# Kernel tuning notes

Hardware: AMD Instinct MI355X
Metric: run time of the kernel (lower is better)

Reference implementation:

```python
import jax, jax.numpy as jnp
import numpy as np

N, T, D, H = 4, 2048, 512, 8
HD = D // H  # head dim = split size


def setup_inputs() -> dict:
    key = jax.random.key(0)
    k1, k2, k3, k4 = jax.random.split(key, 4)
    scale = 1.0 / np.sqrt(D)
    return {
        "query": jax.random.normal(k1, (N, T, D), dtype=jnp.float32),
        "Wk": jax.random.normal(k2, (D, D), dtype=jnp.float32) * scale,
        "Wv": jax.random.normal(k3, (D, D), dtype=jnp.float32) * scale,
        "Wo": jax.random.normal(k4, (D, D), dtype=jnp.float32) * scale,
    }


def reference(query, Wk, Wv, Wo):
    # torch.nn.Linear(x) == x @ W.T (no bias)
    querys = query                              # [N, T, D]
    keys = query @ Wk.T + query                 # residual-added keys [N, T, D]
    values = query @ Wv.T                       # [N, T, D]

    # split along feature dim into H heads, stacked on a leading head axis
    def split_heads(x):
        # [N, T, D] -> [H, N, T, HD]
        return jnp.transpose(x.reshape(N, T, H, HD), (2, 0, 1, 3))

    q = split_heads(querys)
    k = split_heads(keys)
    v = split_heads(values)

    scores = jnp.einsum("hnqd,hnkd->hnqk", q, k) / np.sqrt(HD).astype(np.float32)
    scores = jax.nn.softmax(scores, axis=3)      # [H, N, Tq, Tk]
    out = jnp.einsum("hnqk,hnkd->hnqd", scores, v)

    # concat heads back along feature dim: [H, N, T, HD] -> [N, T, D]
    out = jnp.transpose(out, (1, 2, 0, 3)).reshape(N, T, D)
    out = out @ Wo.T
    return out
```

## Files before the change

kernel.cpp:

```cpp
#include <hip/hip_runtime.h>
#include <cstdint>
#include <cstddef>

#define NB 4
#define TS 2048
#define DM 512
#define HN 8
#define HD 64

typedef __attribute__((ext_vector_type(8))) short bf16x8;
typedef __attribute__((ext_vector_type(16))) float f32x16;
typedef __attribute__((ext_vector_type(4))) float f32x4;
typedef __attribute__((ext_vector_type(4))) short short4v;
typedef __attribute__((ext_vector_type(4))) unsigned u32x4;

static __device__ __forceinline__ short f2bf(float f) {
  unsigned u = __float_as_uint(f);
  unsigned r = (u + 0x7fffu + ((u >> 16) & 1u)) >> 16;
  return (short)r;
}

static __device__ __forceinline__ float bf2f(short s) {
  return __uint_as_float(((unsigned)(unsigned short)s) << 16);
}

static __device__ __forceinline__ unsigned cvtpk(float lo, float hi) {
  unsigned r;
  asm("v_cvt_pk_bf16_f32 %0, %1, %2" : "=v"(r) : "v"(lo), "v"(hi));
  return r;
}

static __device__ __forceinline__ void plane32swap(unsigned& x, unsigned& y) {
  asm volatile("v_permlane32_swap_b32 %0, %1" : "+v"(x), "+v"(y));
}

static __device__ __forceinline__ void gload16(const void* g, void* l) {
  __builtin_amdgcn_global_load_lds(
      (const __attribute__((address_space(1))) void*)g,
      (__attribute__((address_space(3))) void*)l, 16, 0, 0);
}

#define WAIT_VM(N) asm volatile("s_waitcnt vmcnt(" #N ")" ::: "memory")
#define BAR() __builtin_amdgcn_s_barrier()

#define MFMA16(a, b, c) __builtin_amdgcn_mfma_f32_16x16x32_bf16((a), (b), (c), 0, 0, 0)
#define MFMA32(a, b, c) __builtin_amdgcn_mfma_f32_32x32x16_bf16((a), (b), (c), 0, 0, 0)

__global__ __launch_bounds__(256) void cast_all(const float* __restrict__ Q,
                                                const float* __restrict__ Wk,
                                                const float* __restrict__ Wv,
                                                const float* __restrict__ Wo,
                                                short* __restrict__ Qb,
                                                short* __restrict__ Wb) {
  int i = blockIdx.x * 256 + threadIdx.x;
  const int Q4 = (NB * TS * DM) / 4;
  const float* src;
  short* dst;
  int off;
  if (i < Q4) {
    src = Q; dst = Qb; off = i;
  } else {
    int j = i - Q4;
    int which = j >> 16;
    off = j & 65535;
    src = which == 0 ? Wk : (which == 1 ? Wv : Wo);
    dst = Wb + ((size_t)which << 18);
  }
  float4 v = reinterpret_cast<const float4*>(src)[off];
  short4v o;
  o.x = f2bf(v.x);
  o.y = f2bf(v.y);
  o.z = f2bf(v.z);
  o.w = f2bf(v.w);
  reinterpret_cast<short4v*>(dst)[off] = o;
}

template <int MODE>
__global__ __launch_bounds__(256) void gemm512(const short* __restrict__ A,
                                               const short* __restrict__ W,
                                               const float* __restrict__ resid,
                                               void* __restrict__ out0) {
  __shared__ alignas(16) short lA[2][128 * 32];
  __shared__ alignas(16) short lB[2][64 * 32];
  const int row0 = blockIdx.x * 128;
  const int col0 = blockIdx.y * 64;
  const int tid = threadIdx.x;
  const int lane = tid & 63;
  const int wave = tid >> 6;
  const int wr = wave >> 1, wc = wave & 1;
  const int fr = lane & 15, fk = (lane >> 4) * 8;

  f32x4 acc[4][2];
  const f32x4 z4 = {0.f, 0.f, 0.f, 0.f};
#pragma unroll
  for (int m = 0; m < 4; ++m)
#pragma unroll
    for (int nn = 0; nn < 2; ++nn) acc[m][nn] = z4;

  const int sr = tid >> 2;
  const int sc8 = (tid & 3) * 8;

#define GSTAGE(buf, kt)                                                \
  do {                                                                 \
    gload16(&A[(size_t)(row0 + sr) * DM + (kt) + sc8],                 \
            (char*)&lA[(buf)][0] + (size_t)tid * 16);                  \
    gload16(&A[(size_t)(row0 + 64 + sr) * DM + (kt) + sc8],            \
            (char*)&lA[(buf)][0] + 4096 + (size_t)tid * 16);           \
    gload16(&W[(size_t)(col0 + sr) * DM + (kt) + sc8],                 \
            (char*)&lB[(buf)][0] + (size_t)tid * 16);                  \
  } while (0)

  GSTAGE(0, 0);
  __syncthreads();
  int cur = 0;
  for (int kt = 0; kt < 16; ++kt) {
    if (kt < 15) GSTAGE(cur ^ 1, (kt + 1) * 32);
    bf16x8 af[4], bfr[2];
#pragma unroll
    for (int m = 0; m < 4; ++m)
      af[m] = *reinterpret_cast<const bf16x8*>(&lA[cur][(wr * 64 + m * 16 + fr) * 32 + fk]);
#pragma unroll
    for (int nn = 0; nn < 2; ++nn)
      bfr[nn] = *reinterpret_cast<const bf16x8*>(&lB[cur][(wc * 32 + nn * 16 + fr) * 32 + fk]);
    __builtin_amdgcn_s_setprio(1);
#pragma unroll
    for (int m = 0; m < 4; ++m)
#pragma unroll
      for (int nn = 0; nn < 2; ++nn) acc[m][nn] = MFMA16(af[m], bfr[nn], acc[m][nn]);
    __builtin_amdgcn_s_setprio(0);
    __syncthreads();
    cur ^= 1;
  }
#undef GSTAGE

#pragma unroll
  for (int m = 0; m < 4; ++m) {
#pragma unroll
    for (int nn = 0; nn < 2; ++nn) {
#pragma unroll
      for (int i = 0; i < 4; ++i) {
        int gr = row0 + wr * 64 + m * 16 + (lane >> 4) * 4 + i;
        int gc = col0 + wc * 32 + nn * 16 + fr;
        float v = acc[m][nn][i];
        if (MODE == 0) {
          v += resid[(size_t)gr * DM + gc];
          reinterpret_cast<short*>(out0)[(size_t)gr * DM + gc] = f2bf(v);
        } else if (MODE == 1) {
          int nb = gc >> 11, t = gc & (TS - 1);
          reinterpret_cast<short*>(out0)[((size_t)nb * DM + gr) * TS + t] = f2bf(v);
        } else {
          reinterpret_cast<float*>(out0)[(size_t)gr * DM + gc] = v;
        }
      }
    }
  }
}

__global__ __launch_bounds__(512, 4) void attn(const short* __restrict__ Qb,
                                               const short* __restrict__ Kb,
                                               const short* __restrict__ Vt,
                                               short* __restrict__ Ob) {
  __shared__ alignas(16) short kv[2][2][64 * 64];
  const int bid = blockIdx.x;
  const int blk = (bid & 7) * 64 + (bid >> 3);
  const int qt = blk & 15;
  const int nh = blk >> 4;
  const int h = nh & (HN - 1);
  const int n = nh >> 3;
  const int wv = threadIdx.x >> 6, lane = threadIdx.x & 63;
  const int grp = wv >> 2, qs = wv & 3;
  const int l31 = lane & 31, hf = lane >> 5;
  const int q0 = qt * 128 + qs * 32;
  const float SC2 = 0.18033688011f;

  bf16x8 qf[4];
  const short* qrow = Qb + (size_t)(n * TS + q0 + l31) * DM + h * HD;
#pragma unroll
  for (int ks = 0; ks < 4; ++ks) {
    bf16x8 t = *reinterpret_cast<const bf16x8*>(qrow + ks * 16 + hf * 8);
#pragma unroll
    for (int j = 0; j < 8; ++j) t[j] = f2bf(bf2f(t[j]) * SC2);
    qf[ks] = t;
  }

  bf16x8 ones;
#pragma unroll
  for (int i = 0; i < 8; ++i) ones[i] = (short)0x3F80;

  f32x16 o0, o1, osum;
#pragma unroll
  for (int r = 0; r < 16; ++r) {
    o0[r] = 0.f;
    o1[r] = 0.f;
    osum[r] = 0.f;
  }

  const int srow8 = lane >> 3;
  const int scol = ((lane & 7) ^ srow8) * 8;
  const int swz = (l31 & 7) << 4;
  const int tbase = grp * 16;

#define STAGE(t)                                                                      \
  do {                                                                                \
    int r0_ = qs * 16 + srow8;                                                        \
    int r1_ = r0_ + 8;                                                                \
    char* kb_ = (char*)&kv[grp][0][0] + qs * 2048;                                    \
    char* vb_ = (char*)&kv[grp][1][0] + qs * 2048;                                    \
    gload16(Kb + (size_t)(n * TS + (t) * 64 + r0_) * DM + h * HD + scol, kb_);        \
    gload16(Kb + (size_t)(n * TS + (t) * 64 + r1_) * DM + h * HD + scol, kb_ + 1024); \
    gload16(Vt + ((size_t)(nh * HD + r0_) * TS + (t) * 64 + scol), vb_);              \
    gload16(Vt + ((size_t)(nh * HD + r1_) * TS + (t) * 64 + scol), vb_ + 1024);       \
  } while (0)

  STAGE(tbase);

  for (int j = 0; j < 16; ++j) {
    WAIT_VM(0);
    BAR();

    const char* Kl = (const char*)&kv[grp][0][0];
    const char* Vl = (const char*)&kv[grp][1][0];

    f32x16 s0, s1;
#pragma unroll
    for (int r = 0; r < 16; ++r) {
      s0[r] = 0.f;
      s1[r] = 0.f;
    }
    __builtin_amdgcn_s_setprio(1);
#pragma unroll
    for (int ks = 0; ks < 4; ++ks) {
      int colb = ks * 32 + hf * 16;
      bf16x8 ka0 = *reinterpret_cast<const bf16x8*>(Kl + l31 * 128 + (colb ^ swz));
      bf16x8 ka1 = *reinterpret_cast<const bf16x8*>(Kl + (l31 + 32) * 128 + (colb ^ swz));
      s0 = MFMA32(ka0, qf[ks], s0);
      s1 = MFMA32(ka1, qf[ks], s1);
    }
    __builtin_amdgcn_s_setprio(0);

#pragma unroll
    for (int r = 0; r < 16; ++r) {
      s0[r] = __builtin_amdgcn_exp2f(s0[r]);
      s1[r] = __builtin_amdgcn_exp2f(s1[r]);
    }

    unsigned w0[4][2], w1[4][2];
#pragma unroll
    for (int c = 0; c < 4; ++c) {
      w0[c][0] = cvtpk(s0[4 * c], s0[4 * c + 1]);
      w0[c][1] = cvtpk(s0[4 * c + 2], s0[4 * c + 3]);
      w1[c][0] = cvtpk(s1[4 * c], s1[4 * c + 1]);
      w1[c][1] = cvtpk(s1[4 * c + 2], s1[4 * c + 3]);
    }

    __builtin_amdgcn_s_setprio(1);
#pragma unroll
    for (int ks = 0; ks < 4; ++ks) {
      const int ce = (ks & 1) * 2, co = ce + 1;
      unsigned xa = (ks < 2) ? w0[ce][0] : w1[ce][0];
      unsigned xb = (ks < 2) ? w0[ce][1] : w1[ce][1];
      unsigned ya = (ks < 2) ? w0[co][0] : w1[co][0];
      unsigned yb = (ks < 2) ? w0[co][1] : w1[co][1];
      plane32swap(xa, ya);
      plane32swap(xb, yb);
      u32x4 pw;
      pw.x = xa;
      pw.y = xb;
      pw.z = ya;
      pw.w = yb;
      bf16x8 pa = *reinterpret_cast<bf16x8*>(&pw);

      int colb = ks * 32 + hf * 16;
      bf16x8 v0 = *reinterpret_cast<const bf16x8*>(Vl + l31 * 128 + (colb ^ swz));
      bf16x8 v1 = *reinterpret_cast<const bf16x8*>(Vl + (l31 + 32) * 128 + (colb ^ swz));
      o0 = MFMA32(pa, v0, o0);
      o1 = MFMA32(pa, v1, o1);
      osum = MFMA32(pa, ones, osum);
    }
    __builtin_amdgcn_s_setprio(0);

    BAR();
    if (j < 15) STAGE(tbase + j + 1);
  }
#undef STAGE

  __syncthreads();
  float* sp = (float*)&kv[0][0][0];
  const int sbase = (qs * 64 + lane) * 17;
  if (grp == 1) {
#pragma unroll
    for (int r = 0; r < 16; ++r) sp[sbase + r] = o0[r];
  }
  __syncthreads();
  if (grp == 0) {
#pragma unroll
    for (int r = 0; r < 16; ++r) o0[r] += sp[sbase + r];
  }
  __syncthreads();
  if (grp == 1) {
#pragma unroll
    for (int r = 0; r < 16; ++r) sp[sbase + r] = o1[r];
  }
  __syncthreads();
  if (grp == 0) {
#pragma unroll
    for (int r = 0; r < 16; ++r) o1[r] += sp[sbase + r];
  }
  __syncthreads();
  if (grp == 1) {
#pragma unroll
    for (int r = 0; r < 16; ++r) sp[sbase + r] = osum[r];
  }
  __syncthreads();
  if (grp == 0) {
#pragma unroll
    for (int r = 0; r < 16; ++r) osum[r] += sp[sbase + r];
#pragma unroll
    for (int r = 0; r < 16; ++r) {
      int q = q0 + (r & 3) + 8 * (r >> 2) + 4 * hf;
      float is = 1.0f / osum[r];
      size_t base = (size_t)(n * TS + q) * DM + h * HD;
      Ob[base + l31] = f2bf(o0[r] * is);
      Ob[base + 32 + l31] = f2bf(o1[r] * is);
    }
  }
}

extern "C" void kernel_launch(void* const* d_in, const int* in_sizes, int n_in,
                              void* d_out, int out_size, void* d_ws, size_t ws_size,
                              hipStream_t stream) {
  (void)in_sizes; (void)n_in; (void)out_size; (void)ws_size;
  const float* Q = (const float*)d_in[0];
  const float* Wk = (const float*)d_in[1];
  const float* Wv = (const float*)d_in[2];
  const float* Wo = (const float*)d_in[3];

  const size_t QE = (size_t)NB * TS * DM;
  const size_t WE = (size_t)DM * DM;
  short* ws = (short*)d_ws;
  short* Qb = ws;
  short* Kb = Qb + QE;
  short* Vt = Kb + QE;
  short* Ao = Vt + QE;
  short* Wkb = Ao + QE;
  short* Wvb = Wkb + WE;
  short* Wob = Wvb + WE;

  {
    int total4 = (int)((QE + 3 * WE) / 4);
    cast_all<<<total4 / 256, 256, 0, stream>>>(Q, Wk, Wv, Wo, Qb, Wkb);
  }
  {
    dim3 g(64, 8);
    gemm512<0><<<g, 256, 0, stream>>>(Qb, Wkb, Q, (void*)Kb);
  }
  {
    dim3 g(4, 128);
    gemm512<1><<<g, 256, 0, stream>>>(Wvb, Qb, nullptr, (void*)Vt);
  }
  attn<<<NB * HN * (TS / 128), 512, 0, stream>>>(Qb, Kb, Vt, Ao);
  {
    dim3 g(64, 8);
    gemm512<2><<<g, 256, 0, stream>>>(Ao, Wob, nullptr, d_out);
  }
}
```

Before: 88.88 us.

## Fuse K and V projections into one GEMM and double-buffer attention K/V tiles

Merges the separate K and V projection GEMMs into one kernel that loads each Q tile once and computes both products, writing V in transposed layout directly. This removes one launch and one full pass over Qb. The attention kernel now double-buffers its K/V shared-memory tiles so the next tile's global loads overlap the current tile's compute, at the cost of twice the LDS footprint (64KB per block), which may cut occupancy. The cross-group reduction at the end also packs o0, o1 and osum into a single shared-memory exchange, dropping several barriers.

```diff
diff --git a/kernel.cpp b/kernel.cpp
--- a/kernel.cpp
+++ b/kernel.cpp
@@ -75,11 +75,107 @@
   reinterpret_cast<short4v*>(dst)[off] = o;
 }
 
-template <int MODE>
-__global__ __launch_bounds__(256) void gemm512(const short* __restrict__ A,
-                                               const short* __restrict__ W,
+__global__ __launch_bounds__(256) void gemm_kv(const short* __restrict__ Qb,
+                                               const short* __restrict__ Wkb,
+                                               const short* __restrict__ Wvb,
                                                const float* __restrict__ resid,
-                                               void* __restrict__ out0) {
+                                               short* __restrict__ Kb,
+                                               short* __restrict__ Vt) {
+  __shared__ alignas(16) short lA[2][128 * 32];
+  __shared__ alignas(16) short lK[2][64 * 32];
+  __shared__ alignas(16) short lV[2][64 * 32];
+  const int row0 = blockIdx.x * 128;
+  const int col0 = blockIdx.y * 64;
+  const int tid = threadIdx.x;
+  const int lane = tid & 63;
+  const int wave = tid >> 6;
+  const int wr = wave >> 1, wc = wave & 1;
+  const int fr = lane & 15, fk = (lane >> 4) * 8;
+
+  f32x4 kacc[4][2], vacc[2][4];
+  const f32x4 z4 = {0.f, 0.f, 0.f, 0.f};
+#pragma unroll
+  for (int m = 0; m < 4; ++m)
+#pragma unroll
+    for (int nn = 0; nn < 2; ++nn) {
+      kacc[m][nn] = z4;
+      vacc[nn][m] = z4;
+    }
+
+  const int sr = tid >> 2;
+  const int sc8 = (tid & 3) * 8;
+
+#define GSTAGE(buf, kt)                                                 \
+  do {                                                                  \
+    gload16(&Qb[(size_t)(row0 + sr) * DM + (kt) + sc8],                 \
+            (char*)&lA[(buf)][0] + (size_t)tid * 16);                   \
+    gload16(&Qb[(size_t)(row0 + 64 + sr) * DM + (kt) + sc8],            \
+            (char*)&lA[(buf)][0] + 4096 + (size_t)tid * 16);            \
+    gload16(&Wkb[(size_t)(col0 + sr) * DM + (kt) + sc8],                \
+            (char*)&lK[(buf)][0] + (size_t)tid * 16);                   \
+    gload16(&Wvb[(size_t)(col0 + sr) * DM + (kt) + sc8],                \
+            (char*)&lV[(buf)][0] + (size_t)tid * 16);                   \
+  } while (0)
+
+  GSTAGE(0, 0);
+  __syncthreads();
+  int cur = 0;
+  for (int kt = 0; kt < 16; ++kt) {
+    if (kt < 15) GSTAGE(cur ^ 1, (kt + 1) * 32);
+    bf16x8 af[4], bk[2], bv[2];
+#pragma unroll
+    for (int m = 0; m < 4; ++m)
+      af[m] = *reinterpret_cast<const bf16x8*>(&lA[cur][(wr * 64 + m * 16 + fr) * 32 + fk]);
+#pragma unroll
+    for (int nn = 0; nn < 2; ++nn) {
+      bk[nn] = *reinterpret_cast<const bf16x8*>(&lK[cur][(wc * 32 + nn * 16 + fr) * 32 + fk]);
+      bv[nn] = *reinterpret_cast<const bf16x8*>(&lV[cur][(wc * 32 + nn * 16 + fr) * 32 + fk]);
+    }
+    __builtin_amdgcn_s_setprio(1);
+#pragma unroll
+    for (int m = 0; m < 4; ++m)
+#pragma unroll
+      for (int nn = 0; nn < 2; ++nn) {
+        kacc[m][nn] = MFMA16(af[m], bk[nn], kacc[m][nn]);
+        vacc[nn][m] = MFMA16(bv[nn], af[m], vacc[nn][m]);
+      }
+    __builtin_amdgcn_s_setprio(0);
+    __syncthreads();
+    cur ^= 1;
+  }
+#undef GSTAGE
+
+#pragma unroll
+  for (int m = 0; m < 4; ++m) {
+#pragma unroll
+    for (int nn = 0; nn < 2; ++nn) {
+#pragma unroll
+      for (int i = 0; i < 4; ++i) {
+        int gr = row0 + wr * 64 + m * 16 + (lane >> 4) * 4 + i;
+        int gc = col0 + wc * 32 + nn * 16 + fr;
+        float v = kacc[m][nn][i] + resid[(size_t)gr * DM + gc];
+        Kb[(size_t)gr * DM + gc] = f2bf(v);
+      }
+    }
+  }
+#pragma unroll
+  for (int nn = 0; nn < 2; ++nn) {
+#pragma unroll
+    for (int m = 0; m < 4; ++m) {
+#pragma unroll
+      for (int i = 0; i < 4; ++i) {
+        int d = col0 + wc * 32 + nn * 16 + (lane >> 4) * 4 + i;
+        int q = row0 + wr * 64 + m * 16 + fr;
+        int nb = q >> 11, t = q & (TS - 1);
+        Vt[((size_t)nb * DM + d) * TS + t] = f2bf(vacc[nn][m][i]);
+      }
+    }
+  }
+}
+
+__global__ __launch_bounds__(256) void gemm_o(const short* __restrict__ A,
+                                              const short* __restrict__ W,
+                                              float* __restrict__ out0) {
   __shared__ alignas(16) short lA[2][128 * 32];
   __shared__ alignas(16) short lB[2][64 * 32];
   const int row0 = blockIdx.x * 128;
@@ -134,33 +230,22 @@
 #undef GSTAGE
 
 #pragma unroll
-  for (int m = 0; m < 4; ++m) {
-#pragma unroll
-    for (int nn = 0; nn < 2; ++nn) {
+  for (int m = 0; m < 4; ++m)
+#pragma unroll
+    for (int nn = 0; nn < 2; ++nn)
 #pragma unroll
       for (int i = 0; i < 4; ++i) {
         int gr = row0 + wr * 64 + m * 16 + (lane >> 4) * 4 + i;
         int gc = col0 + wc * 32 + nn * 16 + fr;
-        float v = acc[m][nn][i];
-        if (MODE == 0) {
-          v += resid[(size_t)gr * DM + gc];
-          reinterpret_cast<short*>(out0)[(size_t)gr * DM + gc] = f2bf(v);
-        } else if (MODE == 1) {
-          int nb = gc >> 11, t = gc & (TS - 1);
-          reinterpret_cast<short*>(out0)[((size_t)nb * DM + gr) * TS + t] = f2bf(v);
-        } else {
-          reinterpret_cast<float*>(out0)[(size_t)gr * DM + gc] = v;
-        }
+        out0[(size_t)gr * DM + gc] = acc[m][nn][i];
       }
-    }
-  }
 }
 
 __global__ __launch_bounds__(512, 4) void attn(const short* __restrict__ Qb,
                                                const short* __restrict__ Kb,
                                                const short* __restrict__ Vt,
                                                short* __restrict__ Ob) {
-  __shared__ alignas(16) short kv[2][2][64 * 64];
+  __shared__ alignas(16) short kv[2][2][2][64 * 64];
   const int bid = blockIdx.x;
   const int blk = (bid & 7) * 64 + (bid >> 3);
   const int qt = blk & 15;
@@ -200,26 +285,32 @@
   const int swz = (l31 & 7) << 4;
   const int tbase = grp * 16;
 
-#define STAGE(t)                                                                      \
+#define STAGE(buf, t)                                                                 \
   do {                                                                                \
     int r0_ = qs * 16 + srow8;                                                        \
     int r1_ = r0_ + 8;                                                                \
-    char* kb_ = (char*)&kv[grp][0][0] + qs * 2048;                                    \
-    char* vb_ = (char*)&kv[grp][1][0] + qs * 2048;                                    \
+    char* kb_ = (char*)&kv[grp][(buf)][0][0] + qs * 2048;                             \
+    char* vb_ = (char*)&kv[grp][(buf)][1][0] + qs * 2048;                             \
     gload16(Kb + (size_t)(n * TS + (t) * 64 + r0_) * DM + h * HD + scol, kb_);        \
     gload16(Kb + (size_t)(n * TS + (t) * 64 + r1_) * DM + h * HD + scol, kb_ + 1024); \
     gload16(Vt + ((size_t)(nh * HD + r0_) * TS + (t) * 64 + scol), vb_);              \
     gload16(Vt + ((size_t)(nh * HD + r1_) * TS + (t) * 64 + scol), vb_ + 1024);       \
   } while (0)
 
-  STAGE(tbase);
-
+  STAGE(0, tbase);
+
+  int cur = 0;
   for (int j = 0; j < 16; ++j) {
-    WAIT_VM(0);
+    if (j < 15) {
+      STAGE(cur ^ 1, tbase + j + 1);
+      WAIT_VM(4);
+    } else {
+      WAIT_VM(0);
+    }
     BAR();
 
-    const char* Kl = (const char*)&kv[grp][0][0];
-    const char* Vl = (const char*)&kv[grp][1][0];
+    const char* Kl = (const char*)&kv[grp][cur][0][0];
+    const char* Vl = (const char*)&kv[grp][cur][1][0];
 
     f32x16 s0, s1;
 #pragma unroll
@@ -280,41 +371,28 @@
     __builtin_amdgcn_s_setprio(0);
 
     BAR();
-    if (j < 15) STAGE(tbase + j + 1);
+    cur ^= 1;
   }
 #undef STAGE
 
-  __syncthreads();
-  float* sp = (float*)&kv[0][0][0];
-  const int sbase = (qs * 64 + lane) * 17;
+  float* sp = (float*)&kv[0][0][0][0];
+  const int sbase = (qs * 64 + lane) * 49;
   if (grp == 1) {
 #pragma unroll
-    for (int r = 0; r < 16; ++r) sp[sbase + r] = o0[r];
+    for (int r = 0; r < 16; ++r) {
+      sp[sbase + r] = o0[r];
+      sp[sbase + 16 + r] = o1[r];
+      sp[sbase + 32 + r] = osum[r];
+    }
   }
   __syncthreads();
   if (grp == 0) {
 #pragma unroll
-    for (int r = 0; r < 16; ++r) o0[r] += sp[sbase + r];
-  }
-  __syncthreads();
-  if (grp == 1) {
-#pragma unroll
-    for (int r = 0; r < 16; ++r) sp[sbase + r] = o1[r];
-  }
-  __syncthreads();
-  if (grp == 0) {
-#pragma unroll
-    for (int r = 0; r < 16; ++r) o1[r] += sp[sbase + r];
-  }
-  __syncthreads();
-  if (grp == 1) {
-#pragma unroll
-    for (int r = 0; r < 16; ++r) sp[sbase + r] = osum[r];
-  }
-  __syncthreads();
-  if (grp == 0) {
-#pragma unroll
-    for (int r = 0; r < 16; ++r) osum[r] += sp[sbase + r];
+    for (int r = 0; r < 16; ++r) {
+      o0[r] += sp[sbase + r];
+      o1[r] += sp[sbase + 16 + r];
+      osum[r] += sp[sbase + 32 + r];
+    }
 #pragma unroll
     for (int r = 0; r < 16; ++r) {
       int q = q0 + (r & 3) + 8 * (r >> 2) + 4 * hf;
@@ -352,15 +430,11 @@
   }
   {
     dim3 g(64, 8);
-    gemm512<0><<<g, 256, 0, stream>>>(Qb, Wkb, Q, (void*)Kb);
-  }
-  {
-    dim3 g(4, 128);
-    gemm512<1><<<g, 256, 0, stream>>>(Wvb, Qb, nullptr, (void*)Vt);
+    gemm_kv<<<g, 256, 0, stream>>>(Qb, Wkb, Wvb, Q, Kb, Vt);
   }
   attn<<<NB * HN * (TS / 128), 512, 0, stream>>>(Qb, Kb, Vt, Ao);
   {
     dim3 g(64, 8);
-    gemm512<2><<<g, 256, 0, stream>>>(Ao, Wob, nullptr, d_out);
-  }
-}
+    gemm_o<<<g, 256, 0, stream>>>(Ao, Wob, (float*)d_out);
+  }
+}
```

Result: faster. 86.36 us (-2.8%).
